# Performance work log

Measured on AMD Instinct MI355X. Metric: run time of the kernel, lower is better.

Reference implementation:

```python
import jax, jax.numpy as jnp
import numpy as np

INF, OUTF, BIT, GROUPSIZE = 4096, 11008, 4, 128
GROUPS = INF // GROUPSIZE  # 32
PACK = 32 // BIT           # 8 values per int32


def setup_inputs() -> dict:
    key = jax.random.key(0)
    k1, k2, k3, k4, k5 = jax.random.split(key, 5)
    x = jax.random.normal(k1, (2, 2048, INF), dtype=jnp.float32)
    # packed 4-bit weights: (INF*BIT/32, OUTF) int32
    qweight = jax.random.randint(k2, (INF * BIT // 32, OUTF), 0, 2147483647, dtype=jnp.int32)
    scales = jax.random.uniform(k3, (OUTF, GROUPS, 1), dtype=jnp.float32) * 0.01 + 0.001
    zeros = jax.random.uniform(k4, (OUTF, GROUPS, 1), dtype=jnp.float32) * 0.1
    bias = jax.random.normal(k5, (OUTF,), dtype=jnp.float32)
    return {"x": x, "qweight": qweight, "scales": scales, "zeros": zeros, "bias": bias}


def _dequant(qweight, scales, zeros):
    # unpack 8 nibbles per int32 row -> intweight (INF, OUTF)
    shifts = (BIT * jnp.arange(PACK, dtype=jnp.int32))[None, :, None]  # (1,8,1)
    nibbles = (qweight[:, None, :] >> shifts) & 0xF                    # (INF/8, 8, OUTF)
    wq = nibbles.reshape(INF, OUTF).astype(jnp.float32)
    # per-group dequant: W[k,n] = q*scale[n, k//gs] - zero[n, k//gs]
    s = scales[:, :, 0].T[:, None, :]  # (GROUPS, 1, OUTF)
    z = zeros[:, :, 0].T[:, None, :]
    w = wq.reshape(GROUPS, GROUPSIZE, OUTF) * s - z
    return w.reshape(INF, OUTF)


def reference(x, qweight, scales, zeros, bias):
    w = _dequant(qweight, scales, zeros)  # (INF, OUTF)
    # y = x @ W + bias  (matches y init to bias then vecquant4matmul accumulate)
    return jnp.einsum('bsk,kn->bsn', x, w) + bias
```

## Files before the change

kernel.cpp:

```cpp
#include <hip/hip_runtime.h>
#include <hip/hip_bf16.h>
#include <cstdint>
#include <cstddef>

#define K_DIM   4096
#define N_DIM   11008
#define M_DIM   4096
#define GROUPS  32
#define QROWS   512

typedef __bf16 bf16x8 __attribute__((ext_vector_type(8)));
typedef float  f32x4  __attribute__((ext_vector_type(4)));

__device__ __forceinline__ void async16(const void* g, void* lds) {
    __builtin_amdgcn_global_load_lds(
        (const __attribute__((address_space(1))) uint32_t*)g,
        (__attribute__((address_space(3))) uint32_t*)lds,
        16, 0, 0);
}

#define FENCE() asm volatile("" ::: "memory")
#define BAR()   do { FENCE(); __builtin_amdgcn_s_barrier(); FENCE(); } while (0)

#define DQ_NN   64
#define DQ_KK   32
#define DQ_ROW  264
__global__ __launch_bounds__(256) void dequant_kernel(
        const uint32_t* __restrict__ qw,
        const float* __restrict__ scales,
        const float* __restrict__ zeros,
        __bf16* __restrict__ Wt) {
    __shared__ __align__(16) __bf16 T[DQ_NN * DQ_ROW];

    const int n0  = blockIdx.x * DQ_NN;
    const int kk0 = blockIdx.y * DQ_KK;
    const int tid = threadIdx.x;

#pragma unroll
    for (int it = 0; it < 8; ++it) {
        const int flat = it * 256 + tid;
        const int kk_l = flat >> 6;
        const int n_l  = flat & 63;
        const int kk   = kk0 + kk_l;
        const int n    = n0 + n_l;
        const uint32_t q = qw[(size_t)kk * N_DIM + n];
        const int g = kk >> 4;
        const float s = scales[(size_t)n * GROUPS + g];
        const float z = zeros[(size_t)n * GROUPS + g];
        bf16x8 w;
#pragma unroll
        for (int j = 0; j < 8; ++j) {
            float v = (float)((q >> (4 * j)) & 0xF) * s - z;
            w[j] = (__bf16)v;
        }
        *(bf16x8*)(&T[n_l * DQ_ROW + kk_l * 8]) = w;
    }
    __syncthreads();

#pragma unroll
    for (int it = 0; it < 8; ++it) {
        const int flat = it * 256 + tid;
        const int n_l    = flat >> 5;
        const int kchunk = flat & 31;
        bf16x8 v = *(const bf16x8*)(&T[n_l * DQ_ROW + kchunk * 8]);
        *(bf16x8*)(Wt + (size_t)(n0 + n_l) * K_DIM + (size_t)kk0 * 8 + kchunk * 8) = v;
    }
}

__global__ __launch_bounds__(256) void xconv_kernel(
        const float* __restrict__ x, __bf16* __restrict__ xb) {
    const size_t i = ((size_t)blockIdx.x * 256 + threadIdx.x) * 8;
    const float4* p = (const float4*)(x + i);
    float4 a = p[0];
    float4 b = p[1];
    bf16x8 o;
    o[0] = (__bf16)a.x; o[1] = (__bf16)a.y; o[2] = (__bf16)a.z; o[3] = (__bf16)a.w;
    o[4] = (__bf16)b.x; o[5] = (__bf16)b.y; o[6] = (__bf16)b.z; o[7] = (__bf16)b.w;
    *(bf16x8*)(xb + i) = o;
}

#define BM 256
#define BN 256
#define BK 64
#define NT 43
#define MT 16
#define NWG (NT*MT)

#define PH_BODY(MF)                                                           \
    do {                                                                      \
        bf16x8 aLk0 = *(const bf16x8*)(ar0 + (MF)*1024);                      \
        bf16x8 aLk1 = *(const bf16x8*)(ar1 + (MF)*1024);                      \
        bf16x8 aHk0 = *(const bf16x8*)(ar0 + ((MF)+1)*1024);                  \
        bf16x8 aHk1 = *(const bf16x8*)(ar1 + ((MF)+1)*1024);                  \
        BAR();                                                                \
        __builtin_amdgcn_s_setprio(1);                                        \
        acc[(MF)  ][0] = __builtin_amdgcn_mfma_f32_16x16x32_bf16(aLk0, b0k0, acc[(MF)  ][0], 0,0,0); \
        acc[(MF)  ][1] = __builtin_amdgcn_mfma_f32_16x16x32_bf16(aLk0, b1k0, acc[(MF)  ][1], 0,0,0); \
        acc[(MF)  ][2] = __builtin_amdgcn_mfma_f32_16x16x32_bf16(aLk0, b2k0, acc[(MF)  ][2], 0,0,0); \
        acc[(MF)  ][3] = __builtin_amdgcn_mfma_f32_16x16x32_bf16(aLk0, b3k0, acc[(MF)  ][3], 0,0,0); \
        acc[(MF)+1][0] = __builtin_amdgcn_mfma_f32_16x16x32_bf16(aHk0, b0k0, acc[(MF)+1][0], 0,0,0); \
        acc[(MF)+1][1] = __builtin_amdgcn_mfma_f32_16x16x32_bf16(aHk0, b1k0, acc[(MF)+1][1], 0,0,0); \
        acc[(MF)+1][2] = __builtin_amdgcn_mfma_f32_16x16x32_bf16(aHk0, b2k0, acc[(MF)+1][2], 0,0,0); \
        acc[(MF)+1][3] = __builtin_amdgcn_mfma_f32_16x16x32_bf16(aHk0, b3k0, acc[(MF)+1][3], 0,0,0); \
        acc[(MF)  ][0] = __builtin_amdgcn_mfma_f32_16x16x32_bf16(aLk1, b0k1, acc[(MF)  ][0], 0,0,0); \
        acc[(MF)  ][1] = __builtin_amdgcn_mfma_f32_16x16x32_bf16(aLk1, b1k1, acc[(MF)  ][1], 0,0,0); \
        acc[(MF)  ][2] = __builtin_amdgcn_mfma_f32_16x16x32_bf16(aLk1, b2k1, acc[(MF)  ][2], 0,0,0); \
        acc[(MF)  ][3] = __builtin_amdgcn_mfma_f32_16x16x32_bf16(aLk1, b3k1, acc[(MF)  ][3], 0,0,0); \
        acc[(MF)+1][0] = __builtin_amdgcn_mfma_f32_16x16x32_bf16(aHk1, b0k1, acc[(MF)+1][0], 0,0,0); \
        acc[(MF)+1][1] = __builtin_amdgcn_mfma_f32_16x16x32_bf16(aHk1, b1k1, acc[(MF)+1][1], 0,0,0); \
        acc[(MF)+1][2] = __builtin_amdgcn_mfma_f32_16x16x32_bf16(aHk1, b2k1, acc[(MF)+1][2], 0,0,0); \
        acc[(MF)+1][3] = __builtin_amdgcn_mfma_f32_16x16x32_bf16(aHk1, b3k1, acc[(MF)+1][3], 0,0,0); \
        __builtin_amdgcn_s_setprio(0);                                        \
    } while (0)

template<bool DO_STAGE>
__device__ __forceinline__ void kgroup(
        const __bf16* __restrict__ ar0, const __bf16* __restrict__ ar1,
        const __bf16* __restrict__ br0, const __bf16* __restrict__ br1,
        const __bf16* (&gsrc)[8], __bf16* lds, const int (&ldst)[8],
        const int soff, f32x4 (&acc)[8][4])
{
    asm volatile("s_waitcnt vmcnt(2)" ::: "memory");
    BAR();
    bf16x8 b0k0 = *(const bf16x8*)(br0 + 0*1024);
    bf16x8 b1k0 = *(const bf16x8*)(br0 + 1*1024);
    bf16x8 b2k0 = *(const bf16x8*)(br0 + 2*1024);
    bf16x8 b3k0 = *(const bf16x8*)(br0 + 3*1024);
    bf16x8 b0k1 = *(const bf16x8*)(br1 + 0*1024);
    bf16x8 b1k1 = *(const bf16x8*)(br1 + 1*1024);
    bf16x8 b2k1 = *(const bf16x8*)(br1 + 2*1024);
    bf16x8 b3k1 = *(const bf16x8*)(br1 + 3*1024);
    if constexpr (DO_STAGE) {
#pragma unroll
        for (int j = 0; j < 8; ++j)
            async16(gsrc[j], lds + ldst[j] + soff);
    }
    PH_BODY(0);
    BAR();
    PH_BODY(2);
    if constexpr (DO_STAGE) { asm volatile("s_waitcnt vmcnt(8)" ::: "memory"); }
    else                    { asm volatile("s_waitcnt vmcnt(0)" ::: "memory"); }
    BAR();
    PH_BODY(4);
    BAR();
    PH_BODY(6);
    if constexpr (DO_STAGE) {
#pragma unroll
        for (int j = 0; j < 8; ++j) gsrc[j] += BK;
    }
}

__global__ __launch_bounds__(512, 2) void gemm_kernel(
        const __bf16* __restrict__ A,
        const __bf16* __restrict__ Bt,
        const float* __restrict__ bias,
        float* __restrict__ C) {
    __shared__ __align__(16) __bf16 lds[65536];

    const int tid  = threadIdx.x;
    const int wave = tid >> 6;
    const int lane = tid & 63;
    const int wm   = wave >> 2;
    const int wn   = wave & 3;
    const int quad = lane >> 4;
    const int l16  = lane & 15;

    const int bid = blockIdx.x;
    const int swz = (bid & 7) * (NWG / 8) + (bid >> 3);
    const int n_t = swz >> 4;
    const int m_t = swz & 15;
    const int m0 = m_t << 8;
    const int n0 = n_t << 8;

    f32x4 acc[8][4] = {};

    const int srow = tid >> 3;
    const int scol = ((tid & 7) ^ (srow & 7)) << 3;

    const __bf16* gsrc[8];
    gsrc[0] = A  + (size_t)(m0 +   0 + srow) * K_DIM + scol;
    gsrc[1] = A  + (size_t)(m0 + 128 + srow) * K_DIM + scol;
    gsrc[2] = Bt + (size_t)(n0 +   0 + srow) * K_DIM + scol;
    gsrc[3] = Bt + (size_t)(n0 +  64 + srow) * K_DIM + scol;
    gsrc[4] = Bt + (size_t)(n0 + 128 + srow) * K_DIM + scol;
    gsrc[5] = Bt + (size_t)(n0 + 192 + srow) * K_DIM + scol;
    gsrc[6] = A  + (size_t)(m0 +  64 + srow) * K_DIM + scol;
    gsrc[7] = A  + (size_t)(m0 + 192 + srow) * K_DIM + scol;

    const int wq = wave << 9;
    const int ldst[8] = {
        0*4096 + wq,          2*4096 + wq,
        32768 + 0*4096 + wq,  32768 + 1*4096 + wq,
        32768 + 2*4096 + wq,  32768 + 3*4096 + wq,
        1*4096 + wq,          3*4096 + wq
    };

#pragma unroll
    for (int j = 0; j < 8; ++j) async16(gsrc[j], lds + ldst[j]);
#pragma unroll
    for (int j = 0; j < 8; ++j) gsrc[j] += BK;

    const int h3  = l16 & 7;
    const int cc0 = (quad ^ h3) << 3;
    const int cc1 = ((quad ^ h3) ^ 4) << 3;
    const int arow = (wm << 7) + l16;
    const int brow = (wn << 6) + l16;

    const __bf16* a00 = lds + arow * 64 + cc0;
    const __bf16* a01 = lds + arow * 64 + cc1;
    const __bf16* b00 = lds + 32768 + brow * 64 + cc0;
    const __bf16* b01 = lds + 32768 + brow * 64 + cc1;

#pragma unroll 1
    for (int gg = 0; gg < 31; ++gg) {
        kgroup<true>(a00,         a01,         b00,         b01,
                     gsrc, lds, ldst, 16384, acc);
        kgroup<true>(a00 + 16384, a01 + 16384, b00 + 16384, b01 + 16384,
                     gsrc, lds, ldst, 0,     acc);
    }
    kgroup<true >(a00,         a01,         b00,         b01,
                  gsrc, lds, ldst, 16384, acc);
    kgroup<false>(a00 + 16384, a01 + 16384, b00 + 16384, b01 + 16384,
                  gsrc, lds, ldst, 0,     acc);

#pragma unroll
    for (int nf = 0; nf < 4; ++nf) {
        const int n = n0 + (wn << 6) + (nf << 4) + l16;
        const float bv = bias[n];
#pragma unroll
        for (int mf = 0; mf < 8; ++mf) {
            const int mrow = m0 + (wm << 7) + (mf << 4) + (quad << 2);
            float* cp = C + (size_t)mrow * N_DIM + n;
#pragma unroll
            for (int r = 0; r < 4; ++r)
                cp[(size_t)r * N_DIM] = acc[mf][nf][r] + bv;
        }
    }
}

extern "C" void kernel_launch(void* const* d_in, const int* in_sizes, int n_in,
                              void* d_out, int out_size, void* d_ws, size_t ws_size,
                              hipStream_t stream) {
    const float*    x      = (const float*)d_in[0];
    const uint32_t* qw     = (const uint32_t*)d_in[1];
    const float*    scales = (const float*)d_in[2];
    const float*    zeros  = (const float*)d_in[3];
    const float*    bias   = (const float*)d_in[4];
    float*          out    = (float*)d_out;

    __bf16* Wt = (__bf16*)d_ws;
    __bf16* xb = (__bf16*)((char*)d_ws + (size_t)N_DIM * K_DIM * sizeof(__bf16));

    dim3 dq_grid(N_DIM / DQ_NN, QROWS / DQ_KK);
    dequant_kernel<<<dq_grid, 256, 0, stream>>>(qw, scales, zeros, Wt);
    xconv_kernel<<<(M_DIM * K_DIM) / (256 * 8), 256, 0, stream>>>(x, xb);

    gemm_kernel<<<NWG, 512, 0, stream>>>(xb, Wt, bias, out);
}
```

Before: 617.0 us.

## Restructure k-group into four phases with interleaved async loads and fewer live registers

The inner k-group is reordered so each phase loads four A fragments and one k-half of B, then issues 16 MFMAs, instead of holding both k-halves of B at once. The eight async global-to-LDS copies are spread two per phase rather than issued together at the start, with the vmcnt waits adjusted to match. This lowers live VGPR pressure and spreads memory traffic across the compute phases, but it reloads A fragments per k-half and changes the barrier pattern, which could add LDS traffic or stalls.

After: 603.1 us. 1.02x faster.

```diff
diff --git a/kernel.cpp b/kernel.cpp
--- a/kernel.cpp
+++ b/kernel.cpp
@@ -86,32 +86,11 @@
 #define MT 16
 #define NWG (NT*MT)
 
-#define PH_BODY(MF)                                                           \
-    do {                                                                      \
-        bf16x8 aLk0 = *(const bf16x8*)(ar0 + (MF)*1024);                      \
-        bf16x8 aLk1 = *(const bf16x8*)(ar1 + (MF)*1024);                      \
-        bf16x8 aHk0 = *(const bf16x8*)(ar0 + ((MF)+1)*1024);                  \
-        bf16x8 aHk1 = *(const bf16x8*)(ar1 + ((MF)+1)*1024);                  \
-        BAR();                                                                \
-        __builtin_amdgcn_s_setprio(1);                                        \
-        acc[(MF)  ][0] = __builtin_amdgcn_mfma_f32_16x16x32_bf16(aLk0, b0k0, acc[(MF)  ][0], 0,0,0); \
-        acc[(MF)  ][1] = __builtin_amdgcn_mfma_f32_16x16x32_bf16(aLk0, b1k0, acc[(MF)  ][1], 0,0,0); \
-        acc[(MF)  ][2] = __builtin_amdgcn_mfma_f32_16x16x32_bf16(aLk0, b2k0, acc[(MF)  ][2], 0,0,0); \
-        acc[(MF)  ][3] = __builtin_amdgcn_mfma_f32_16x16x32_bf16(aLk0, b3k0, acc[(MF)  ][3], 0,0,0); \
-        acc[(MF)+1][0] = __builtin_amdgcn_mfma_f32_16x16x32_bf16(aHk0, b0k0, acc[(MF)+1][0], 0,0,0); \
-        acc[(MF)+1][1] = __builtin_amdgcn_mfma_f32_16x16x32_bf16(aHk0, b1k0, acc[(MF)+1][1], 0,0,0); \
-        acc[(MF)+1][2] = __builtin_amdgcn_mfma_f32_16x16x32_bf16(aHk0, b2k0, acc[(MF)+1][2], 0,0,0); \
-        acc[(MF)+1][3] = __builtin_amdgcn_mfma_f32_16x16x32_bf16(aHk0, b3k0, acc[(MF)+1][3], 0,0,0); \
-        acc[(MF)  ][0] = __builtin_amdgcn_mfma_f32_16x16x32_bf16(aLk1, b0k1, acc[(MF)  ][0], 0,0,0); \
-        acc[(MF)  ][1] = __builtin_amdgcn_mfma_f32_16x16x32_bf16(aLk1, b1k1, acc[(MF)  ][1], 0,0,0); \
-        acc[(MF)  ][2] = __builtin_amdgcn_mfma_f32_16x16x32_bf16(aLk1, b2k1, acc[(MF)  ][2], 0,0,0); \
-        acc[(MF)  ][3] = __builtin_amdgcn_mfma_f32_16x16x32_bf16(aLk1, b3k1, acc[(MF)  ][3], 0,0,0); \
-        acc[(MF)+1][0] = __builtin_amdgcn_mfma_f32_16x16x32_bf16(aHk1, b0k1, acc[(MF)+1][0], 0,0,0); \
-        acc[(MF)+1][1] = __builtin_amdgcn_mfma_f32_16x16x32_bf16(aHk1, b1k1, acc[(MF)+1][1], 0,0,0); \
-        acc[(MF)+1][2] = __builtin_amdgcn_mfma_f32_16x16x32_bf16(aHk1, b2k1, acc[(MF)+1][2], 0,0,0); \
-        acc[(MF)+1][3] = __builtin_amdgcn_mfma_f32_16x16x32_bf16(aHk1, b3k1, acc[(MF)+1][3], 0,0,0); \
-        __builtin_amdgcn_s_setprio(0);                                        \
-    } while (0)
+#define MFMA4(AV, R)                                                          \
+    acc[(R)][0] = __builtin_amdgcn_mfma_f32_16x16x32_bf16((AV), b0, acc[(R)][0], 0,0,0); \
+    acc[(R)][1] = __builtin_amdgcn_mfma_f32_16x16x32_bf16((AV), b1, acc[(R)][1], 0,0,0); \
+    acc[(R)][2] = __builtin_amdgcn_mfma_f32_16x16x32_bf16((AV), b2, acc[(R)][2], 0,0,0); \
+    acc[(R)][3] = __builtin_amdgcn_mfma_f32_16x16x32_bf16((AV), b3, acc[(R)][3], 0,0,0);
 
 template<bool DO_STAGE>
 __device__ __forceinline__ void kgroup(
@@ -120,30 +99,75 @@
         const __bf16* (&gsrc)[8], __bf16* lds, const int (&ldst)[8],
         const int soff, f32x4 (&acc)[8][4])
 {
+    bf16x8 a0, a1, a2, a3, b0, b1, b2, b3;
+
     asm volatile("s_waitcnt vmcnt(2)" ::: "memory");
     BAR();
-    bf16x8 b0k0 = *(const bf16x8*)(br0 + 0*1024);
-    bf16x8 b1k0 = *(const bf16x8*)(br0 + 1*1024);
-    bf16x8 b2k0 = *(const bf16x8*)(br0 + 2*1024);
-    bf16x8 b3k0 = *(const bf16x8*)(br0 + 3*1024);
-    bf16x8 b0k1 = *(const bf16x8*)(br1 + 0*1024);
-    bf16x8 b1k1 = *(const bf16x8*)(br1 + 1*1024);
-    bf16x8 b2k1 = *(const bf16x8*)(br1 + 2*1024);
-    bf16x8 b3k1 = *(const bf16x8*)(br1 + 3*1024);
-    if constexpr (DO_STAGE) {
-#pragma unroll
-        for (int j = 0; j < 8; ++j)
-            async16(gsrc[j], lds + ldst[j] + soff);
-    }
-    PH_BODY(0);
-    BAR();
-    PH_BODY(2);
-    if constexpr (DO_STAGE) { asm volatile("s_waitcnt vmcnt(8)" ::: "memory"); }
+    a0 = *(const bf16x8*)(ar0 + 0*1024);
+    a1 = *(const bf16x8*)(ar0 + 1*1024);
+    a2 = *(const bf16x8*)(ar0 + 2*1024);
+    a3 = *(const bf16x8*)(ar0 + 3*1024);
+    b0 = *(const bf16x8*)(br0 + 0*1024);
+    b1 = *(const bf16x8*)(br0 + 1*1024);
+    b2 = *(const bf16x8*)(br0 + 2*1024);
+    b3 = *(const bf16x8*)(br0 + 3*1024);
+    if constexpr (DO_STAGE) {
+        async16(gsrc[0], lds + ldst[0] + soff);
+        async16(gsrc[1], lds + ldst[1] + soff);
+    }
+    BAR();
+    __builtin_amdgcn_s_setprio(1);
+    MFMA4(a0, 0) MFMA4(a1, 1) MFMA4(a2, 2) MFMA4(a3, 3)
+    __builtin_amdgcn_s_setprio(0);
+
+    if constexpr (DO_STAGE) { asm volatile("s_waitcnt vmcnt(2)" ::: "memory"); }
     else                    { asm volatile("s_waitcnt vmcnt(0)" ::: "memory"); }
     BAR();
-    PH_BODY(4);
-    BAR();
-    PH_BODY(6);
+    a0 = *(const bf16x8*)(ar0 + 4*1024);
+    a1 = *(const bf16x8*)(ar0 + 5*1024);
+    a2 = *(const bf16x8*)(ar0 + 6*1024);
+    a3 = *(const bf16x8*)(ar0 + 7*1024);
+    if constexpr (DO_STAGE) {
+        async16(gsrc[2], lds + ldst[2] + soff);
+        async16(gsrc[3], lds + ldst[3] + soff);
+    }
+    BAR();
+    __builtin_amdgcn_s_setprio(1);
+    MFMA4(a0, 4) MFMA4(a1, 5) MFMA4(a2, 6) MFMA4(a3, 7)
+    __builtin_amdgcn_s_setprio(0);
+
+    BAR();
+    a0 = *(const bf16x8*)(ar1 + 0*1024);
+    a1 = *(const bf16x8*)(ar1 + 1*1024);
+    a2 = *(const bf16x8*)(ar1 + 2*1024);
+    a3 = *(const bf16x8*)(ar1 + 3*1024);
+    b0 = *(const bf16x8*)(br1 + 0*1024);
+    b1 = *(const bf16x8*)(br1 + 1*1024);
+    b2 = *(const bf16x8*)(br1 + 2*1024);
+    b3 = *(const bf16x8*)(br1 + 3*1024);
+    if constexpr (DO_STAGE) {
+        async16(gsrc[4], lds + ldst[4] + soff);
+        async16(gsrc[5], lds + ldst[5] + soff);
+    }
+    BAR();
+    __builtin_amdgcn_s_setprio(1);
+    MFMA4(a0, 0) MFMA4(a1, 1) MFMA4(a2, 2) MFMA4(a3, 3)
+    __builtin_amdgcn_s_setprio(0);
+
+    BAR();
+    a0 = *(const bf16x8*)(ar1 + 4*1024);
+    a1 = *(const bf16x8*)(ar1 + 5*1024);
+    a2 = *(const bf16x8*)(ar1 + 6*1024);
+    a3 = *(const bf16x8*)(ar1 + 7*1024);
+    if constexpr (DO_STAGE) {
+        async16(gsrc[6], lds + ldst[6] + soff);
+        async16(gsrc[7], lds + ldst[7] + soff);
+    }
+    BAR();
+    __builtin_amdgcn_s_setprio(1);
+    MFMA4(a0, 4) MFMA4(a1, 5) MFMA4(a2, 6) MFMA4(a3, 7)
+    __builtin_amdgcn_s_setprio(0);
+
     if constexpr (DO_STAGE) {
 #pragma unroll
         for (int j = 0; j < 8; ++j) gsrc[j] += BK;
```
